# Kernel tuning notes

Measured on AMD Instinct MI355X. Metric: run time of the kernel, lower is better.

Reference implementation:

```python
import jax, jax.numpy as jnp
import numpy as np

VOCAB = 14
D_MODEL = 1024
D_FF = 4096
B, S = 8, 2048
EPS = 1e-5


def _linear_params(key, d_in, d_out):
    kw, kb = jax.random.split(key)
    lim = 1.0 / np.sqrt(d_in)
    W = jax.random.uniform(kw, (d_out, d_in), jnp.float32, -lim, lim)
    b = jax.random.uniform(kb, (d_out,), jnp.float32, -lim, lim)
    return W, b


def setup_inputs() -> dict:
    key = jax.random.key(0)
    ks = jax.random.split(key, 8)
    x = jax.random.randint(ks[0], (B, S), 0, VOCAB)
    tok_emb = jax.random.normal(ks[1], (VOCAB, D_MODEL), jnp.float32)
    qw, qb = _linear_params(ks[2], D_MODEL, D_MODEL)
    kw, kb = _linear_params(ks[3], D_MODEL, D_MODEL)
    vw, vb = _linear_params(ks[4], D_MODEL, D_MODEL)
    pw, pb = _linear_params(ks[5], D_MODEL, D_MODEL)
    f1w, f1b = _linear_params(ks[6], D_MODEL, D_FF)
    f2w, f2b = _linear_params(ks[7], D_FF, D_MODEL)
    ones = jnp.ones((D_MODEL,), jnp.float32)
    zeros = jnp.zeros((D_MODEL,), jnp.float32)
    return {
        "x": x, "tok_emb": tok_emb,
        "ln1_w": ones, "ln1_b": zeros,
        "qw": qw, "qb": qb, "kw": kw, "kb": kb, "vw": vw, "vb": vb,
        "pw": pw, "pb": pb,
        "ln2_w": ones, "ln2_b": zeros,
        "f1w": f1w, "f1b": f1b, "f2w": f2w, "f2b": f2b,
        "lnf_w": ones, "lnf_b": zeros,
    }


def _layernorm(h, w, b):
    mu = jnp.mean(h, axis=-1, keepdims=True)
    var = jnp.var(h, axis=-1, keepdims=True)
    return (h - mu) / jnp.sqrt(var + EPS) * w + b


def reference(x, tok_emb, ln1_w, ln1_b, qw, qb, kw, kb, vw, vb, pw, pb,
              ln2_w, ln2_b, f1w, f1b, f2w, f2b, lnf_w, lnf_b):
    h = tok_emb[x]                                  # [B,S,D]
    r = h
    hn = _layernorm(h, ln1_w, ln1_b)
    q = hn @ qw.T + qb
    k = hn @ kw.T + kb
    v = hn @ vw.T + vb
    scale = 1.0 / jnp.sqrt(jnp.float32(q.shape[-1]))
    att = jnp.einsum('bqd,bkd->bqk', q, k) * scale  # [B,S,S]
    causal = jnp.tril(jnp.ones((S, S), bool))
    att = jnp.where(causal, att, -jnp.inf)
    att = jax.nn.softmax(att, axis=-1)
    h = jnp.einsum('bqk,bkd->bqd', att, v) @ pw.T + pb
    h = r + h
    r2 = h
    hn = _layernorm(h, ln2_w, ln2_b)
    h = jax.nn.gelu(hn @ f1w.T + f1b, approximate=False) @ f2w.T + f2b
    h = r2 + h
    h = _layernorm(h, lnf_w, lnf_b)
    logits = h @ tok_emb.T                          # [B,S,VOCAB]
    return logits
```

## Files before the change

### kernel.cpp

```cpp
#include <hip/hip_runtime.h>
#include <math.h>

typedef unsigned short u16;
typedef __attribute__((ext_vector_type(8))) short short8;
typedef __attribute__((ext_vector_type(8))) __bf16 bf16x8;
typedef __attribute__((ext_vector_type(4))) float f32x4;

#define FLAG_BIAS   1
#define FLAG_RES    2
#define FLAG_GELU   4
#define FLAG_TRI    8
#define FLAG_CK     16

__device__ __forceinline__ u16 f2bf(float f) {
  unsigned u = __builtin_bit_cast(unsigned, f);
  unsigned r = u + 0x7fffu + ((u >> 16) & 1u);
  return (u16)(r >> 16);
}
__device__ __forceinline__ float bf2f(u16 u) {
  return __builtin_bit_cast(float, (unsigned)u << 16);
}
__device__ __forceinline__ float wred_sum(float v) {
#pragma unroll
  for (int m = 32; m; m >>= 1) v += __shfl_xor(v, m, 64);
  return v;
}
__device__ __forceinline__ float wred_max(float v) {
#pragma unroll
  for (int m = 32; m; m >>= 1) v = fmaxf(v, __shfl_xor(v, m, 64));
  return v;
}
__device__ __forceinline__ float gelu_fast(float x) {
  float y = 0.7978845608f * x * (1.f + 0.044715f * x * x);
  float e = __expf(2.f * y);
  float th = 1.f - 2.f / (e + 1.f);
  return 0.5f * x * (1.f + th);
}
__device__ __forceinline__ f32x4 mfma16(short8 a, short8 b, f32x4 c) {
  return __builtin_amdgcn_mfma_f32_16x16x32_bf16(
      __builtin_bit_cast(bf16x8, a), __builtin_bit_cast(bf16x8, b), c, 0, 0, 0);
}

#define GLOAD_LDS16(gptr, lptr)                                              \
  __builtin_amdgcn_global_load_lds(                                          \
      (const __attribute__((address_space(1))) void*)(gptr),                 \
      (__attribute__((address_space(3))) void*)(lptr), 16, 0, 0)

__global__ __launch_bounds__(512, 2) void gemm256(
    const u16* __restrict__ Aptr, const u16* __restrict__ Bptr,
    u16* __restrict__ Cptr, const float* __restrict__ bias,
    const u16* __restrict__ resp,
    int M, int N, int K, int lda, int ldb, int ldc, float alpha, int flags,
    long long sA, long long sB, long long sC) {
  const int nwg = gridDim.x;
  const int cpx = nwg >> 3;
  const int bid = blockIdx.x;
  const int swz = (bid & 7) * cpx + (bid >> 3);
  int bm, bn, z;
  if (flags & FLAG_TRI) {
    z = swz / 36;
    int tq = swz - z * 36;
    bm = (int)((sqrtf(8.f * tq + 1.f) - 1.f) * 0.5f);
    while ((bm + 1) * (bm + 2) / 2 <= tq) ++bm;
    while (bm * (bm + 1) / 2 > tq) --bm;
    bn = tq - bm * (bm + 1) / 2;
  } else {
    z = blockIdx.z;
    const int nbm = M >> 8;
    bn = swz / nbm;
    bm = swz - bn * nbm;
  }
  const int gm0 = bm << 8, gn0 = bn << 8;
  const int kend = (flags & FLAG_CK) ? min(K, gm0 + 256) : K;
  const int NT = kend >> 5;

  __shared__ __align__(16) u16 As[4][256 * 32];
  __shared__ __align__(16) u16 Bs[4][256 * 32];

  const int t = threadIdx.x;
  const int l = t & 63;
  const int w = t >> 6;
  const int wr = w >> 2, wc = w & 3;
  const int frow = l & 15;
  const int g4 = l >> 4;

  const int srow = (w << 4) + (l >> 2);
  const int sch = (l & 3) ^ ((srow >> 1) & 3);
  const u16* Ag = Aptr + (size_t)z * sA + (size_t)(gm0 + srow) * lda + sch * 8;
  const u16* Bg = Bptr + (size_t)z * sB + (size_t)(gn0 + srow) * ldb + sch * 8;
  const long long a128 = (long long)128 * lda, b128 = (long long)128 * ldb;

  auto STAGE_A = [&](int buf, int kt) {
    GLOAD_LDS16(Ag + kt, &As[buf][w * 512]);
    GLOAD_LDS16(Ag + a128 + kt, &As[buf][4096 + w * 512]);
  };
  auto STAGE_B = [&](int buf, int kt) {
    GLOAD_LDS16(Bg + kt, &Bs[buf][w * 512]);
    GLOAD_LDS16(Bg + b128 + kt, &Bs[buf][4096 + w * 512]);
  };

  f32x4 acc[8][4] = {};

  STAGE_A(0, 0); STAGE_B(0, 0);
  STAGE_A(1, 32); STAGE_B(1, 32);
  asm volatile("s_waitcnt vmcnt(4)" ::: "memory");
  __builtin_amdgcn_s_barrier();
  __builtin_amdgcn_sched_barrier(0);

  for (int tt = 0; tt < NT; ++tt) {
    const int buf = tt & 3;
    const int nbuf = (tt + 2) & 3;
    const int kt2 = (tt + 2) << 5;
    const bool pre = (tt + 2) < NT;
    short8 af[4], bf[4];
#pragma unroll
    for (int m = 0; m < 4; ++m) {
      int rr = wr * 128 + m * 16 + frow;
      af[m] = *(const short8*)&As[buf][rr * 32 + ((g4 ^ ((rr >> 1) & 3)) << 3)];
    }
#pragma unroll
    for (int n = 0; n < 4; ++n) {
      int rr = wc * 64 + n * 16 + frow;
      bf[n] = *(const short8*)&Bs[buf][rr * 32 + ((g4 ^ ((rr >> 1) & 3)) << 3)];
    }
    if (pre) STAGE_A(nbuf, kt2);
    __builtin_amdgcn_s_barrier();
    asm volatile("s_waitcnt lgkmcnt(0)" ::: "memory");
    __builtin_amdgcn_sched_barrier(0);
    __builtin_amdgcn_s_setprio(1);
#pragma unroll
    for (int m = 0; m < 4; ++m)
#pragma unroll
      for (int n = 0; n < 4; ++n)
        acc[m][n] = mfma16(af[m], bf[n], acc[m][n]);
    __builtin_amdgcn_s_setprio(0);
    __builtin_amdgcn_sched_barrier(0);
    __builtin_amdgcn_s_barrier();
#pragma unroll
    for (int m = 0; m < 4; ++m) {
      int rr = wr * 128 + 64 + m * 16 + frow;
      af[m] = *(const short8*)&As[buf][rr * 32 + ((g4 ^ ((rr >> 1) & 3)) << 3)];
    }
    if (pre) STAGE_B(nbuf, kt2);
    if (pre) asm volatile("s_waitcnt vmcnt(4)" ::: "memory");
    else     asm volatile("s_waitcnt vmcnt(0)" ::: "memory");
    __builtin_amdgcn_s_barrier();
    asm volatile("s_waitcnt lgkmcnt(0)" ::: "memory");
    __builtin_amdgcn_sched_barrier(0);
    __builtin_amdgcn_s_setprio(1);
#pragma unroll
    for (int m = 0; m < 4; ++m)
#pragma unroll
      for (int n = 0; n < 4; ++n)
        acc[4 + m][n] = mfma16(af[m], bf[n], acc[4 + m][n]);
    __builtin_amdgcn_s_setprio(0);
    __builtin_amdgcn_sched_barrier(0);
    __builtin_amdgcn_s_barrier();
  }

  u16* Cb = Cptr + (size_t)z * sC;
  const bool hasB = flags & FLAG_BIAS, hasR = flags & FLAG_RES;
  const bool doG = flags & FLAG_GELU;
#pragma unroll
  for (int m = 0; m < 8; ++m) {
#pragma unroll
    for (int n = 0; n < 4; ++n) {
      int row0 = gm0 + wr * 128 + m * 16 + ((l >> 4) << 2);
      int col = gn0 + wc * 64 + n * 16 + frow;
      float bv = hasB ? bias[col] : 0.0f;
#pragma unroll
      for (int i = 0; i < 4; ++i) {
        float v = acc[m][n][i] * alpha + bv;
        if (doG) v = gelu_fast(v);
        size_t idx = (size_t)(row0 + i) * ldc + col;
        if (hasR) v += bf2f(resp[idx]);
        Cb[idx] = f2bf(v);
      }
    }
  }
}

__global__ __launch_bounds__(256) void f32_to_bf16_v4(const float* __restrict__ in,
                                                      u16* __restrict__ out, int n4) {
  int i = blockIdx.x * 256 + threadIdx.x;
  if (i < n4) {
    float4 v = ((const float4*)in)[i];
    ushort4 o;
    o.x = f2bf(v.x); o.y = f2bf(v.y); o.z = f2bf(v.z); o.w = f2bf(v.w);
    ((ushort4*)out)[i] = o;
  }
}

__global__ __launch_bounds__(256) void embed_ln1(
    const int* __restrict__ x, const float* __restrict__ emb,
    const float* __restrict__ w, const float* __restrict__ b,
    u16* __restrict__ h16, u16* __restrict__ hn) {
  int row = blockIdx.x * 4 + (threadIdx.x >> 6);
  int lane = threadIdx.x & 63;
  int tok = x[row];
  const float* e = emb + (size_t)tok * 1024;
  float v[16];
  float s = 0.f, q = 0.f;
#pragma unroll
  for (int i = 0; i < 16; ++i) { v[i] = e[lane + i * 64]; s += v[i]; q += v[i] * v[i]; }
  s = wred_sum(s); q = wred_sum(q);
  float mu = s * (1.0f / 1024.0f);
  float rstd = rsqrtf(q * (1.0f / 1024.0f) - mu * mu + 1e-5f);
  u16* hr = h16 + (size_t)row * 1024;
  u16* hnr = hn + (size_t)row * 1024;
#pragma unroll
  for (int i = 0; i < 16; ++i) {
    int d = lane + i * 64;
    hr[d] = f2bf(v[i]);
    hnr[d] = f2bf((v[i] - mu) * rstd * w[d] + b[d]);
  }
}

__global__ __launch_bounds__(256) void ln_rows(
    const u16* __restrict__ in, const float* __restrict__ w,
    const float* __restrict__ b, u16* __restrict__ out) {
  int row = blockIdx.x * 4 + (threadIdx.x >> 6);
  int lane = threadIdx.x & 63;
  const short8* ir = (const short8*)(in + (size_t)row * 1024);
  short8 c0 = ir[lane], c1 = ir[lane + 64];
  float v[16];
  float s = 0.f, q = 0.f;
#pragma unroll
  for (int j = 0; j < 8; ++j) {
    v[j] = bf2f((u16)c0[j]); v[8 + j] = bf2f((u16)c1[j]);
  }
#pragma unroll
  for (int j = 0; j < 16; ++j) { s += v[j]; q += v[j] * v[j]; }
  s = wred_sum(s); q = wred_sum(q);
  float mu = s * (1.0f / 1024.0f);
  float rstd = rsqrtf(q * (1.0f / 1024.0f) - mu * mu + 1e-5f);
  short8 o0, o1;
#pragma unroll
  for (int j = 0; j < 8; ++j) {
    int d0 = lane * 8 + j, d1 = 512 + lane * 8 + j;
    o0[j] = (short)f2bf((v[j] - mu) * rstd * w[d0] + b[d0]);
    o1[j] = (short)f2bf((v[8 + j] - mu) * rstd * w[d1] + b[d1]);
  }
  short8* orow = (short8*)(out + (size_t)row * 1024);
  orow[lane] = o0; orow[lane + 64] = o1;
}

__global__ __launch_bounds__(256) void softmax_causal(u16* att) {
  int r = blockIdx.x * 4 + (threadIdx.x >> 6);
  int lane = threadIdx.x & 63;
  int i = r & 2047;
  int n = i + 1;
  int ng = (i >> 9) + 1;
  short8* pv = (short8*)(att + (size_t)r * 2048);
  float v[32];
  float m = -1e30f;
#pragma unroll
  for (int g = 0; g < 4; ++g) {
    if (g < ng) {
      short8 c = pv[g * 64 + lane];
#pragma unroll
      for (int j = 0; j < 8; ++j) {
        int idx = g * 512 + lane * 8 + j;
        float f = (idx < n) ? bf2f((u16)c[j]) : -1e30f;
        v[g * 8 + j] = f;
        m = fmaxf(m, f);
      }
    }
  }
  m = wred_max(m);
  float s = 0.f;
#pragma unroll
  for (int g = 0; g < 4; ++g) {
    if (g < ng) {
#pragma unroll
      for (int j = 0; j < 8; ++j) {
        int idx = g * 512 + lane * 8 + j;
        float e = (idx < n) ? __expf(v[g * 8 + j] - m) : 0.f;
        v[g * 8 + j] = e; s += e;
      }
    }
  }
  s = wred_sum(s);
  float inv = 1.0f / s;
#pragma unroll
  for (int g = 0; g < 4; ++g) {
    if (g < ng) {
      short8 o;
#pragma unroll
      for (int j = 0; j < 8; ++j) o[j] = (short)f2bf(v[g * 8 + j] * inv);
      pv[g * 64 + lane] = o;
    }
  }
}

__global__ __launch_bounds__(256) void transpose_v(const u16* __restrict__ V,
                                                   u16* __restrict__ Vt, int ldv) {
  int z = blockIdx.z;
  const u16* src = V + (size_t)z * 2048 * ldv;
  u16* dst = Vt + (size_t)z * 1024 * 2048;
  int j0 = (blockIdx.x >> 4) << 6;
  int d0 = (blockIdx.x & 15) << 6;
  __shared__ u16 tile[64][65];
  int c = threadIdx.x & 15;
  int rr = threadIdx.x >> 4;
#pragma unroll
  for (int q = 0; q < 4; ++q) {
    int row = rr + q * 16;
    ushort4 val = *(const ushort4*)(src + (size_t)(j0 + row) * ldv + d0 + c * 4);
    tile[row][c * 4 + 0] = val.x; tile[row][c * 4 + 1] = val.y;
    tile[row][c * 4 + 2] = val.z; tile[row][c * 4 + 3] = val.w;
  }
  __syncthreads();
#pragma unroll
  for (int q = 0; q < 4; ++q) {
    int drow = rr + q * 16;
    ushort4 o;
    o.x = tile[c * 4 + 0][drow]; o.y = tile[c * 4 + 1][drow];
    o.z = tile[c * 4 + 2][drow]; o.w = tile[c * 4 + 3][drow];
    *(ushort4*)(dst + (size_t)(d0 + drow) * 2048 + j0 + c * 4) = o;
  }
}

__global__ __launch_bounds__(256) void lnf_logits(
    const u16* __restrict__ h, const float* __restrict__ w,
    const float* __restrict__ b, const float* __restrict__ emb,
    float* __restrict__ out) {
  __shared__ float el[14 * 1056];
  int t = threadIdx.x;
  for (int f = t * 4; f < 14 * 1024; f += 1024) {
    float4 e = *(const float4*)(emb + f);
    int v = f >> 10, d = f & 1023;
    float* dst = el + v * 1056 + d + (d >> 5);
    dst[0] = e.x; dst[1] = e.y; dst[2] = e.z; dst[3] = e.w;
  }
  __syncthreads();
  int lane = t & 63, wid = t >> 6;
  float w0[8], w1[8], b0[8], b1[8];
#pragma unroll
  for (int j = 0; j < 8; ++j) {
    int d0 = lane * 8 + j, d1 = 512 + lane * 8 + j;
    w0[j] = w[d0]; b0[j] = b[d0];
    w1[j] = w[d1]; b1[j] = b[d1];
  }
  const float* e0 = el + lane * 8 + (lane >> 2);
  const float* e1 = el + 528 + lane * 8 + (lane >> 2);
  for (int rr = 0; rr < 8; ++rr) {
    int row = blockIdx.x * 32 + wid * 8 + rr;
    const short8* hr = (const short8*)(h + (size_t)row * 1024);
    short8 c0 = hr[lane], c1 = hr[lane + 64];
    float v0[8], v1[8];
    float s = 0.f, q = 0.f;
#pragma unroll
    for (int j = 0; j < 8; ++j) {
      v0[j] = bf2f((u16)c0[j]); v1[j] = bf2f((u16)c1[j]);
      s += v0[j] + v1[j];
      q += v0[j] * v0[j] + v1[j] * v1[j];
    }
    s = wred_sum(s); q = wred_sum(q);
    float mu = s * (1.0f / 1024.0f);
    float rstd = rsqrtf(q * (1.0f / 1024.0f) - mu * mu + 1e-5f);
    float h0[8], h1[8];
#pragma unroll
    for (int j = 0; j < 8; ++j) {
      h0[j] = (v0[j] - mu) * rstd * w0[j] + b0[j];
      h1[j] = (v1[j] - mu) * rstd * w1[j] + b1[j];
    }
    float p[14];
#pragma unroll
    for (int v = 0; v < 14; ++v) {
      const float* ev0 = e0 + v * 1056;
      const float* ev1 = e1 + v * 1056;
      float a = 0.f;
#pragma unroll
      for (int j = 0; j < 8; ++j) a += h0[j] * ev0[j] + h1[j] * ev1[j];
      p[v] = a;
    }
#pragma unroll
    for (int m = 32; m; m >>= 1)
#pragma unroll
      for (int v = 0; v < 14; ++v) p[v] += __shfl_xor(p[v], m, 64);
    if (lane == 0) {
      float* orow = out + (size_t)row * 14;
#pragma unroll
      for (int v = 0; v < 14; ++v) orow[v] = p[v];
    }
  }
}

__global__ void zero_out_k(float* o, int n) {
  int i = blockIdx.x * 256 + threadIdx.x;
  if (i < n) o[i] = 0.f;
}
__global__ void diag_k(float* o, float v) { if (threadIdx.x == 0) o[0] = v; }

extern "C" void kernel_launch(void* const* d_in, const int* in_sizes, int n_in,
                              void* d_out, int out_size, void* d_ws, size_t ws_size,
                              hipStream_t stream) {
  const int* x = (const int*)d_in[0];
  const float* tok_emb = (const float*)d_in[1];
  const float* ln1_w = (const float*)d_in[2];
  const float* ln1_b = (const float*)d_in[3];
  const float* qw = (const float*)d_in[4];
  const float* qb = (const float*)d_in[5];
  const float* kw = (const float*)d_in[6];
  const float* kb = (const float*)d_in[7];
  const float* vw = (const float*)d_in[8];
  const float* vb = (const float*)d_in[9];
  const float* pw = (const float*)d_in[10];
  const float* pb = (const float*)d_in[11];
  const float* ln2_w = (const float*)d_in[12];
  const float* ln2_b = (const float*)d_in[13];
  const float* f1w = (const float*)d_in[14];
  const float* f1b = (const float*)d_in[15];
  const float* f2w = (const float*)d_in[16];
  const float* f2b = (const float*)d_in[17];
  const float* lnf_w = (const float*)d_in[18];
  const float* lnf_b = (const float*)d_in[19];
  float* out = (float*)d_out;

  const long long T = 16384, D = 1024, F = 4096, S = 2048;
  const size_t MB = 1ull << 20;
  char* base = (char*)d_ws;

  if (ws_size < 224 * MB) {
    zero_out_k<<<dim3((out_size + 255) / 256), 256, 0, stream>>>(out, out_size);
    diag_k<<<dim3(1), 1, 0, stream>>>(out, (float)ws_size);
    return;
  }

  u16* rA16 = (u16*)base;
  u16* rB   = (u16*)(base + 32 * MB);
  u16* QKV  = (u16*)(base + 64 * MB);
  u16* SC   = (u16*)(base + 160 * MB);
  u16* W3   = SC;
  float* qkvb = (float*)(base + 166 * MB);
  u16* PW  = SC;
  u16* CB  = QKV;
  u16* F1  = (u16*)(base + 192 * MB);
  u16* F2  = (u16*)(base + 200 * MB);

  auto cvt = [&](const float* src, u16* dst, long long n) {
    int n4 = (int)(n / 4);
    f32_to_bf16_v4<<<dim3((n4 + 255) / 256), dim3(256), 0, stream>>>(src, dst, n4);
  };
  auto gemm = [&](const u16* A, const u16* B, u16* C, const float* bias,
                  const u16* res, long long M, long long N, long long K,
                  long long lda, long long ldb, long long ldc, float alpha,
                  int flags, long long sA, long long sB, long long sC,
                  int gx, int gz) {
    gemm256<<<dim3(gx, 1, gz), dim3(512), 0, stream>>>(
        A, B, C, bias, res, (int)M, (int)N, (int)K, (int)lda, (int)ldb,
        (int)ldc, alpha, flags, sA, sB, sC);
  };

  cvt(qw, W3, D * D);
  cvt(kw, W3 + 1024 * 1024, D * D);
  cvt(vw, W3 + 2 * 1024 * 1024, D * D);
  hipMemcpyAsync(qkvb, qb, D * 4, hipMemcpyDeviceToDevice, stream);
  hipMemcpyAsync(qkvb + 1024, kb, D * 4, hipMemcpyDeviceToDevice, stream);
  hipMemcpyAsync(qkvb + 2048, vb, D * 4, hipMemcpyDeviceToDevice, stream);

  embed_ln1<<<dim3(T / 4), 256, 0, stream>>>(x, tok_emb, ln1_w, ln1_b, rA16, rB);

  gemm(rB, W3, QKV, qkvb, nullptr, T, 3072, D, D, D, 3072, 1.f, FLAG_BIAS,
       0, 0, 0, 768, 1);

  gemm(QKV, QKV + 1024, SC, nullptr, nullptr, S, S, D, 3072, 3072, 2048,
       0.03125f, FLAG_TRI, S * 3072, S * 3072, S * S, 288, 1);

  transpose_v<<<dim3(512, 1, 8), 256, 0, stream>>>(QKV + 2048, rB, 3072);

  softmax_causal<<<dim3(T / 4), 256, 0, stream>>>(SC);

  gemm(SC, rB, QKV, nullptr, nullptr, S, D, S, S, S, 3072, 1.f, FLAG_CK,
       S * S, D * S, S * 3072, 32, 8);

  cvt(pw, PW, D * D);
  gemm(QKV, PW, rA16, pb, rA16, T, D, D, 3072, D, D, 1.f, FLAG_BIAS | FLAG_RES,
       0, 0, 0, 256, 1);

  ln_rows<<<dim3(T / 4), 256, 0, stream>>>(rA16, ln2_w, ln2_b, rB);

  cvt(f1w, F1, F * D);
  cvt(f2w, F2, D * F);
  gemm(rB, F1, CB, f1b, nullptr, T, F, D, D, D, F, 1.f, FLAG_BIAS | FLAG_GELU,
       0, 0, 0, 1024, 1);
  gemm(CB, F2, rA16, f2b, rA16, T, D, F, F, F, D, 1.f, FLAG_BIAS | FLAG_RES,
       0, 0, 0, 256, 1);

  lnf_logits<<<dim3(512), 256, 0, stream>>>(rA16, lnf_w, lnf_b, tok_emb, out);
}
```

Measured before the change: 848.6 us.

## Restructure GEMM main loop to process 64-wide K steps in four phases

The GEMM main loop now advances 64 elements of K per iteration, split into four phases that each issue one staged global-to-LDS load for the next iteration while computing half the output tile. The LDS swizzle is simplified to an XOR on row&3, and the staging row mapping now uses the thread index directly. The occupancy hint of 2 blocks per CU is dropped from launch bounds, giving the compiler more register freedom. It assumes K is a multiple of 64, and the changed load mapping or vmcnt accounting could introduce stalls or correctness issues.

```diff
diff --git a/kernel.cpp b/kernel.cpp
--- a/kernel.cpp
+++ b/kernel.cpp
@@ -46,7 +46,7 @@
       (const __attribute__((address_space(1))) void*)(gptr),                 \
       (__attribute__((address_space(3))) void*)(lptr), 16, 0, 0)
 
-__global__ __launch_bounds__(512, 2) void gemm256(
+__global__ __launch_bounds__(512) void gemm256(
     const u16* __restrict__ Aptr, const u16* __restrict__ Bptr,
     u16* __restrict__ Cptr, const float* __restrict__ bias,
     const u16* __restrict__ resp,
@@ -72,7 +72,7 @@
   }
   const int gm0 = bm << 8, gn0 = bn << 8;
   const int kend = (flags & FLAG_CK) ? min(K, gm0 + 256) : K;
-  const int NT = kend >> 5;
+  const int NT = kend >> 6;
 
   __shared__ __align__(16) u16 As[4][256 * 32];
   __shared__ __align__(16) u16 Bs[4][256 * 32];
@@ -83,79 +83,81 @@
   const int wr = w >> 2, wc = w & 3;
   const int frow = l & 15;
   const int g4 = l >> 4;
-
-  const int srow = (w << 4) + (l >> 2);
-  const int sch = (l & 3) ^ ((srow >> 1) & 3);
+  const int rsw = (frow & 3);
+
+  const int srow = t >> 2;
+  const int sch = (t & 3) ^ (srow & 3);
   const u16* Ag = Aptr + (size_t)z * sA + (size_t)(gm0 + srow) * lda + sch * 8;
   const u16* Bg = Bptr + (size_t)z * sB + (size_t)(gn0 + srow) * ldb + sch * 8;
   const long long a128 = (long long)128 * lda, b128 = (long long)128 * ldb;
 
-  auto STAGE_A = [&](int buf, int kt) {
-    GLOAD_LDS16(Ag + kt, &As[buf][w * 512]);
-    GLOAD_LDS16(Ag + a128 + kt, &As[buf][4096 + w * 512]);
+  auto stA = [&](int u, int kk) {
+    const int s = (2 * u + kk) & 3;
+    const int c0 = (u << 6) + (kk << 5);
+    GLOAD_LDS16(Ag + c0, &As[s][w * 512]);
+    GLOAD_LDS16(Ag + a128 + c0, &As[s][4096 + w * 512]);
   };
-  auto STAGE_B = [&](int buf, int kt) {
-    GLOAD_LDS16(Bg + kt, &Bs[buf][w * 512]);
-    GLOAD_LDS16(Bg + b128 + kt, &Bs[buf][4096 + w * 512]);
+  auto stB = [&](int u, int kk) {
+    const int s = (2 * u + kk) & 3;
+    const int c0 = (u << 6) + (kk << 5);
+    GLOAD_LDS16(Bg + c0, &Bs[s][w * 512]);
+    GLOAD_LDS16(Bg + b128 + c0, &Bs[s][4096 + w * 512]);
   };
 
   f32x4 acc[8][4] = {};
-
-  STAGE_A(0, 0); STAGE_B(0, 0);
-  STAGE_A(1, 32); STAGE_B(1, 32);
+  short8 af[4], bf[4];
+
+  stA(0, 0); stB(0, 0); stA(0, 1); stB(0, 1);
   asm volatile("s_waitcnt vmcnt(4)" ::: "memory");
   __builtin_amdgcn_s_barrier();
-  __builtin_amdgcn_sched_barrier(0);
 
   for (int tt = 0; tt < NT; ++tt) {
-    const int buf = tt & 3;
-    const int nbuf = (tt + 2) & 3;
-    const int kt2 = (tt + 2) << 5;
-    const bool pre = (tt + 2) < NT;
-    short8 af[4], bf[4];
-#pragma unroll
-    for (int m = 0; m < 4; ++m) {
-      int rr = wr * 128 + m * 16 + frow;
-      af[m] = *(const short8*)&As[buf][rr * 32 + ((g4 ^ ((rr >> 1) & 3)) << 3)];
-    }
-#pragma unroll
-    for (int n = 0; n < 4; ++n) {
-      int rr = wc * 64 + n * 16 + frow;
-      bf[n] = *(const short8*)&Bs[buf][rr * 32 + ((g4 ^ ((rr >> 1) & 3)) << 3)];
-    }
-    if (pre) STAGE_A(nbuf, kt2);
-    __builtin_amdgcn_s_barrier();
-    asm volatile("s_waitcnt lgkmcnt(0)" ::: "memory");
-    __builtin_amdgcn_sched_barrier(0);
-    __builtin_amdgcn_s_setprio(1);
-#pragma unroll
-    for (int m = 0; m < 4; ++m)
-#pragma unroll
-      for (int n = 0; n < 4; ++n)
-        acc[m][n] = mfma16(af[m], bf[n], acc[m][n]);
-    __builtin_amdgcn_s_setprio(0);
-    __builtin_amdgcn_sched_barrier(0);
-    __builtin_amdgcn_s_barrier();
-#pragma unroll
-    for (int m = 0; m < 4; ++m) {
-      int rr = wr * 128 + 64 + m * 16 + frow;
-      af[m] = *(const short8*)&As[buf][rr * 32 + ((g4 ^ ((rr >> 1) & 3)) << 3)];
-    }
-    if (pre) STAGE_B(nbuf, kt2);
-    if (pre) asm volatile("s_waitcnt vmcnt(4)" ::: "memory");
-    else     asm volatile("s_waitcnt vmcnt(0)" ::: "memory");
-    __builtin_amdgcn_s_barrier();
-    asm volatile("s_waitcnt lgkmcnt(0)" ::: "memory");
-    __builtin_amdgcn_sched_barrier(0);
-    __builtin_amdgcn_s_setprio(1);
-#pragma unroll
-    for (int m = 0; m < 4; ++m)
-#pragma unroll
-      for (int n = 0; n < 4; ++n)
-        acc[4 + m][n] = mfma16(af[m], bf[n], acc[4 + m][n]);
-    __builtin_amdgcn_s_setprio(0);
-    __builtin_amdgcn_sched_barrier(0);
-    __builtin_amdgcn_s_barrier();
+    const bool p1 = (tt + 1) < NT;
+    const int s0 = (2 * tt) & 3, s1 = (2 * tt + 1) & 3;
+
+#pragma unroll
+    for (int ph = 0; ph < 4; ++ph) {
+      const int kk = ph >> 1;
+      const int q = ph & 1;
+      const int sl = kk ? s1 : s0;
+#pragma unroll
+      for (int m = 0; m < 4; ++m) {
+        int rr = wr * 128 + q * 64 + m * 16 + frow;
+        af[m] = *(const short8*)&As[sl][rr * 32 + ((g4 ^ rsw) << 3)];
+      }
+      if (q == 0) {
+#pragma unroll
+        for (int n = 0; n < 4; ++n) {
+          int rr = wc * 64 + n * 16 + frow;
+          bf[n] = *(const short8*)&Bs[sl][rr * 32 + ((g4 ^ rsw) << 3)];
+        }
+      }
+      if (p1) {
+        if (ph == 0) stA(tt + 1, 0);
+        else if (ph == 1) stB(tt + 1, 0);
+        else if (ph == 2) stA(tt + 1, 1);
+        else stB(tt + 1, 1);
+      }
+      __builtin_amdgcn_s_barrier();
+      asm volatile("s_waitcnt lgkmcnt(0)" ::: "memory");
+      __builtin_amdgcn_sched_barrier(0);
+      __builtin_amdgcn_s_setprio(1);
+#pragma unroll
+      for (int m = 0; m < 4; ++m)
+#pragma unroll
+        for (int n = 0; n < 4; ++n)
+          acc[q * 4 + m][n] = mfma16(af[m], bf[n], acc[q * 4 + m][n]);
+      __builtin_amdgcn_s_setprio(0);
+      __builtin_amdgcn_sched_barrier(0);
+      if (ph == 1) {
+        if (p1) asm volatile("s_waitcnt vmcnt(4)" ::: "memory");
+        else    asm volatile("s_waitcnt vmcnt(0)" ::: "memory");
+      } else if (ph == 3) {
+        if (p1) asm volatile("s_waitcnt vmcnt(4)" ::: "memory");
+        else    asm volatile("s_waitcnt vmcnt(0)" ::: "memory");
+      }
+      __builtin_amdgcn_s_barrier();
+    }
   }
 
   u16* Cb = Cptr + (size_t)z * sC;
```

New measurement: 853.6 us. Within noise of the previous version (+0.6%).
